# Kernel tuning notes

Measured on AMD Instinct MI355X. Metric: run time of the kernel, lower is better.

The kernel has to match this reference:

```python
import jax, jax.numpy as jnp
import numpy as np

N_NODES = 50000
N_EDGES = 600000
IN_F, HID, OUT_F = 602, 128, 41


def _gconv(x, W, b, src, dst, n):
    # DGL GraphConv, norm='both': D_dst^{-1/2} A (D_src^{-1/2} x W) + b
    ones = jnp.ones(src.shape, dtype=x.dtype)
    deg_out = jnp.clip(jax.ops.segment_sum(ones, src, num_segments=n), 1.0)
    deg_in = jnp.clip(jax.ops.segment_sum(ones, dst, num_segments=n), 1.0)
    h = x * jax.lax.rsqrt(deg_out)[:, None]
    h = h @ W  # dense transform first (in_feats > out_feats path)
    agg = jax.ops.segment_sum(h[src], dst, num_segments=n)  # [N, out]
    return agg * jax.lax.rsqrt(deg_in)[:, None] + b


def setup_inputs() -> dict:
    key = jax.random.key(0)
    ks = jax.random.split(key, 8)
    features = jax.random.normal(ks[0], (N_NODES, IN_F), dtype=jnp.float32)
    src = jax.random.randint(ks[1], (N_EDGES,), 0, N_NODES, dtype=jnp.int32)
    dst = jax.random.randint(ks[2], (N_EDGES,), 0, N_NODES, dtype=jnp.int32)
    def glorot(k, fan_in, fan_out):
        s = jnp.sqrt(6.0 / (fan_in + fan_out)).astype(jnp.float32)
        return jax.random.uniform(k, (fan_in, fan_out), jnp.float32, -s, s)
    return {
        'features': features, 'src': src, 'dst': dst,
        'W1': glorot(ks[3], IN_F, HID), 'b1': jnp.zeros((HID,), jnp.float32),
        'W2': glorot(ks[4], HID, HID), 'b2': jnp.zeros((HID,), jnp.float32),
        'W3': glorot(ks[5], HID, HID), 'b3': jnp.zeros((HID,), jnp.float32),
        'Wfc': glorot(ks[6], HID, OUT_F), 'bfc': jnp.zeros((OUT_F,), jnp.float32),
    }


def reference(features, src, dst, W1, b1, W2, b2, W3, b3, Wfc, bfc):
    n = features.shape[0]
    relu = jax.nn.relu
    x = relu(_gconv(features, W1, b1, src, dst, n))  # x = _x
    _x = relu(_gconv(x, W2, b2, src, dst, n))        # branch (layer2)
    x = relu(_gconv(x, W2, b2, src, dst, n))         # main (same layer2)
    x = relu(_gconv(x, W3, b3, src, dst, n))         # layer3
    x = relu(x + _x)                                  # residual + relu
    return x @ Wfc + bfc
```

## Files before the change

kernel.cpp:

```cpp
#include <hip/hip_runtime.h>
#include <hip/hip_bf16.h>

#define NN   50000
#define NE   600000
#define INF  602
#define HID  128
#define OUTF 41
#define NBLK 196

#define HISTB 2344
#define GEMMB 782

typedef __attribute__((ext_vector_type(8))) short bf16x8;
typedef __attribute__((ext_vector_type(4))) float f32x4;
typedef __attribute__((ext_vector_type(2))) float f32x2;

__device__ inline unsigned short f2bf(float x) {
    unsigned u = __float_as_uint(x);
    unsigned r = u + 0x7FFF + ((u >> 16) & 1);
    return (unsigned short)(r >> 16);
}

__device__ inline unsigned pack2bf(float lo, float hi) {
    return ((unsigned)f2bf(hi) << 16) | f2bf(lo);
}

__device__ inline f32x2 up2(unsigned u) {
    return (f32x2){__uint_as_float(u << 16), __uint_as_float(u & 0xFFFF0000u)};
}

#define GLL16(gp, lp) \
    __builtin_amdgcn_global_load_lds((const __attribute__((address_space(1))) unsigned int*)(gp), \
                                     (__attribute__((address_space(3))) unsigned int*)(lp), 16, 0, 0)

__device__ inline void prep_w_body(const float* __restrict__ W, int K,
                                   unsigned short* __restrict__ out, int total4, int i) {
    if (i >= total4) return;
    int col = i & 127;
    int k4 = (i >> 7) << 2;
    short4 h;
    h.x = (short)f2bf((k4 + 0 < K) ? W[(size_t)(k4 + 0) * HID + col] : 0.f);
    h.y = (short)f2bf((k4 + 1 < K) ? W[(size_t)(k4 + 1) * HID + col] : 0.f);
    h.z = (short)f2bf((k4 + 2 < K) ? W[(size_t)(k4 + 2) * HID + col] : 0.f);
    h.w = (short)f2bf((k4 + 3 < K) ? W[(size_t)(k4 + 3) * HID + col] : 0.f);
    *(short4*)&out[(size_t)(k4 >> 3) * 1024 + col * 8 + (k4 & 7)] = h;
}

__global__ __launch_bounds__(256) void hist_prep_k(const int* __restrict__ src,
                                                   const int* __restrict__ dst,
                                                   int* __restrict__ cnt_out,
                                                   int* __restrict__ cnt_in,
                                                   const float* __restrict__ W1,
                                                   const float* __restrict__ W2,
                                                   const float* __restrict__ W3,
                                                   unsigned short* __restrict__ W1t,
                                                   unsigned short* __restrict__ W2t,
                                                   unsigned short* __restrict__ W3t) {
    int b = blockIdx.x;
    if (b < HISTB) {
        int e = b * 256 + threadIdx.x;
        if (e < NE) {
            atomicAdd(&cnt_out[src[e]], 1);
            atomicAdd(&cnt_in[dst[e]], 1);
        }
    } else {
        int b2 = b - HISTB;
        if (b2 < 80)       prep_w_body(W1, INF, W1t, 20480, b2 * 256 + threadIdx.x);
        else if (b2 < 96)  prep_w_body(W2, HID, W2t, 4096, (b2 - 80) * 256 + threadIdx.x);
        else               prep_w_body(W3, HID, W3t, 4096, (b2 - 96) * 256 + threadIdx.x);
    }
}

__global__ __launch_bounds__(256) void scan1_k(const int* __restrict__ cnt,
                                               int* __restrict__ rowptr,
                                               int* __restrict__ blockSum) {
    __shared__ int tmp[256];
    int tid = threadIdx.x;
    int i = blockIdx.x * 256 + tid;
    int v = (i < NN) ? cnt[i] : 0;
    tmp[tid] = v;
    __syncthreads();
#pragma unroll
    for (int off = 1; off < 256; off <<= 1) {
        int t = (tid >= off) ? tmp[tid - off] : 0;
        __syncthreads();
        tmp[tid] += t;
        __syncthreads();
    }
    if (i < NN) rowptr[i] = tmp[tid] - v;
    if (tid == 255) blockSum[blockIdx.x] = tmp[255];
}

__global__ __launch_bounds__(256) void scan23_k(int* __restrict__ rowptr,
                                                const int* __restrict__ blockSum,
                                                int* __restrict__ wcur,
                                                const int* __restrict__ cnt_out,
                                                const int* __restrict__ cnt_in,
                                                float* __restrict__ rs_out,
                                                float* __restrict__ rs_in) {
    const int tid = threadIdx.x;
    const int bid = blockIdx.x;
    int vAll = (tid < NBLK) ? blockSum[tid] : 0;
    int vPre = (tid < bid) ? vAll : 0;
#pragma unroll
    for (int o = 32; o; o >>= 1) {
        vAll += __shfl_down(vAll, o);
        vPre += __shfl_down(vPre, o);
    }
    __shared__ int sA[4], sP[4];
    if ((tid & 63) == 0) { sA[tid >> 6] = vAll; sP[tid >> 6] = vPre; }
    __syncthreads();
    int offAll = sA[0] + sA[1] + sA[2] + sA[3];
    int offPre = sP[0] + sP[1] + sP[2] + sP[3];
    int i = bid * 256 + tid;
    if (i < NN) {
        int r = rowptr[i] + offPre;
        rowptr[i] = r;
        wcur[i] = r;
        int co = cnt_out[i]; if (co < 1) co = 1;
        int ci = cnt_in[i];  if (ci < 1) ci = 1;
        rs_out[i] = rsqrtf((float)co);
        rs_in[i]  = rsqrtf((float)ci);
    }
    if (bid == NBLK - 1 && tid == 0) rowptr[NN] = offAll;
}

__global__ __launch_bounds__(256) void fill_gemm1_k(const int* __restrict__ src,
                                                    const int* __restrict__ dst,
                                                    int* __restrict__ wcur,
                                                    int* __restrict__ csrsrc,
                                                    const float* __restrict__ A,
                                                    const unsigned short* __restrict__ Wt,
                                                    const float* __restrict__ rs_out,
                                                    unsigned short* __restrict__ H, int n) {
    if (blockIdx.x < HISTB) {
        int e = blockIdx.x * 256 + threadIdx.x;
        if (e < NE) {
            int p = atomicAdd(&wcur[dst[e]], 1);
            csrsrc[p] = src[e];
        }
        return;
    }

    const int gb = blockIdx.x - HISTB;
    const int tid = threadIdx.x;
    const int wave = tid >> 6;
    const int lane = tid & 63;
    const int quad = lane >> 4;
    const int l16 = lane & 15;
    const int tileBase = gb * 64 + wave * 16;

    const int arow_i = tileBase + l16;
    const float* __restrict__ arow = A + (size_t)(arow_i < n ? arow_i : 0) * INF;

    f32x4 acc[8];
#pragma unroll
    for (int j = 0; j < 8; ++j) acc[j] = (f32x4){0.f, 0.f, 0.f, 0.f};

    auto step = [&](float4& va, float4& vb, int kgUse, int kgRef, bool doRef) {
        union { bf16x8 v; unsigned u[4]; } af;
        af.u[0] = pack2bf(va.x, va.y);
        af.u[1] = pack2bf(va.z, va.w);
        af.u[2] = pack2bf(vb.x, vb.y);
        af.u[3] = pack2bf(vb.z, vb.w);
        if (doRef) {
            const float* p = arow + kgRef * 32 + quad * 8;
            va = *(const float4*)p;
            vb = *(const float4*)(p + 4);
        }
        const unsigned short* bg = Wt + (size_t)(kgUse * 4 + quad) * 1024 + l16 * 8;
#pragma unroll
        for (int nt = 0; nt < 8; ++nt) {
            bf16x8 bf = *(const bf16x8*)(bg + nt * 128);
            acc[nt] = __builtin_amdgcn_mfma_f32_16x16x32_bf16(af.v, bf, acc[nt], 0, 0, 0);
        }
    };

    float4 a0, b0, a1, b1, a2, b2;
    {
        const float* p0 = arow + quad * 8;
        a0 = *(const float4*)p0;            b0 = *(const float4*)(p0 + 4);
        a1 = *(const float4*)(p0 + 32);     b1 = *(const float4*)(p0 + 36);
        a2 = *(const float4*)(p0 + 64);     b2 = *(const float4*)(p0 + 68);
    }
    for (int i = 0; i < 5; ++i) {
        step(a0, b0, 3 * i,     3 * i + 3, true);
        step(a1, b1, 3 * i + 1, 3 * i + 4, true);
        step(a2, b2, 3 * i + 2, 3 * i + 5, true);
    }
    step(a0, b0, 15, 0, false);
    {
        int kb = 576 + quad * 8;
        if (quad < 3) {
            a0 = *(const float4*)(arow + kb);
            b0 = *(const float4*)(arow + kb + 4);
        } else {
            a0 = make_float4(arow[600], arow[601], 0.f, 0.f);
            b0 = make_float4(0.f, 0.f, 0.f, 0.f);
        }
    }
    step(a1, b1, 16, 0, false);
    step(a2, b2, 17, 0, false);
    step(a0, b0, 18, 0, false);

#pragma unroll
    for (int r = 0; r < 4; ++r) {
        int row = tileBase + quad * 4 + r;
        if (row < n) {
            float ro = rs_out[row];
#pragma unroll
            for (int nt = 0; nt < 8; ++nt)
                H[(size_t)row * HID + nt * 16 + l16] = f2bf(acc[nt][r] * ro);
        }
    }
}

__global__ __launch_bounds__(256) void gemm_hid_k(const unsigned short* __restrict__ A,
                                                  const unsigned short* __restrict__ Wt,
                                                  unsigned short* __restrict__ H, int n) {
    __shared__ __attribute__((aligned(16))) short As[64 * 136];
    __shared__ __attribute__((aligned(16))) short Bs[16384];

    const int tid = threadIdx.x;
    const int wave = tid >> 6;
    const int lane = tid & 63;
    const int quad = lane >> 4;
    const int l16 = lane & 15;
    const int wm = wave >> 1;
    const int wn = wave & 1;
    const int rowBase = blockIdx.x * 64;

#pragma unroll
    for (int c = 0; c < 8; ++c)
        GLL16(Wt + c * 2048 + tid * 8, &Bs[c * 2048 + tid * 8]);

#pragma unroll
    for (int c = 0; c < 4; ++c) {
        int f = c * 256 + tid;
        int row = f >> 4;
        int k16 = (f & 15) << 3;
        int grow = rowBase + row;
        int4 v = {0, 0, 0, 0};
        if (grow < n) v = *(const int4*)(A + (size_t)grow * HID + k16);
        *(int4*)&As[row * 136 + k16] = v;
    }
    __syncthreads();

    f32x4 acc[2][4];
#pragma unroll
    for (int i = 0; i < 2; ++i)
#pragma unroll
        for (int j = 0; j < 4; ++j) acc[i][j] = (f32x4){0.f, 0.f, 0.f, 0.f};

#pragma unroll
    for (int kq = 0; kq < 4; ++kq) {
        bf16x8 af[2], bfr[4];
#pragma unroll
        for (int mt = 0; mt < 2; ++mt)
            af[mt] = *(const bf16x8*)&As[(wm * 32 + mt * 16 + l16) * 136 + kq * 32 + quad * 8];
#pragma unroll
        for (int nt = 0; nt < 4; ++nt)
            bfr[nt] = *(const bf16x8*)&Bs[(kq * 4 + quad) * 1024 + (wn * 64 + nt * 16 + l16) * 8];
#pragma unroll
        for (int mt = 0; mt < 2; ++mt)
#pragma unroll
            for (int nt = 0; nt < 4; ++nt)
                acc[mt][nt] = __builtin_amdgcn_mfma_f32_16x16x32_bf16(af[mt], bfr[nt], acc[mt][nt], 0, 0, 0);
    }

#pragma unroll
    for (int mt = 0; mt < 2; ++mt)
#pragma unroll
        for (int r = 0; r < 4; ++r) {
            int row = rowBase + wm * 32 + mt * 16 + quad * 4 + r;
            if (row < n) {
#pragma unroll
                for (int nt = 0; nt < 4; ++nt) {
                    int col = wn * 64 + nt * 16 + l16;
                    H[(size_t)row * HID + col] = f2bf(acc[mt][nt][r]);
                }
            }
        }
}

__global__ __launch_bounds__(256) void gather_k(const unsigned short* __restrict__ H,
                                                const int* __restrict__ rowptr,
                                                const int* __restrict__ csrsrc,
                                                const float* __restrict__ rs_in,
                                                const float* __restrict__ rs_out,
                                                const float* __restrict__ bias,
                                                const float* __restrict__ resid,
                                                float* __restrict__ outX,
                                                unsigned short* __restrict__ outXs,
                                                int n) {
    const int lane = threadIdx.x & 63;
    const int g = lane >> 4;
    const int l = lane & 15;
    const int gbase = g << 4;
    const int wid = blockIdx.x * 4 + (threadIdx.x >> 6);
    const int node = wid * 4 + g;
    const bool alive = node < n;

    int beg = 0, end = 0;
    if (alive) { beg = rowptr[node]; end = rowptr[node + 1]; }

    f32x2 a01 = {0.f, 0.f}, a23 = {0.f, 0.f}, a45 = {0.f, 0.f}, a67 = {0.f, 0.f};

    for (int base = beg; base < end; base += 16) {
        int m = end - base; if (m > 16) m = 16;
        int idx = (l < m) ? csrsrc[base + l] : 0;
        int j = 0;
        for (; j + 3 < m; j += 4) {
            int s0 = __shfl(idx, gbase | j);
            int s1 = __shfl(idx, gbase | (j + 1));
            int s2 = __shfl(idx, gbase | (j + 2));
            int s3 = __shfl(idx, gbase | (j + 3));
            int4 u0 = *(const int4*)(H + (size_t)s0 * HID + l * 8);
            int4 u1 = *(const int4*)(H + (size_t)s1 * HID + l * 8);
            int4 u2 = *(const int4*)(H + (size_t)s2 * HID + l * 8);
            int4 u3 = *(const int4*)(H + (size_t)s3 * HID + l * 8);
#pragma unroll
            for (int q = 0; q < 4; ++q) {
                int4 u = (q == 0) ? u0 : (q == 1) ? u1 : (q == 2) ? u2 : u3;
                a01 += up2((unsigned)u.x);
                a23 += up2((unsigned)u.y);
                a45 += up2((unsigned)u.z);
                a67 += up2((unsigned)u.w);
            }
        }
        for (; j < m; ++j) {
            int s = __shfl(idx, gbase | j);
            int4 u = *(const int4*)(H + (size_t)s * HID + l * 8);
            a01 += up2((unsigned)u.x);
            a23 += up2((unsigned)u.y);
            a45 += up2((unsigned)u.z);
            a67 += up2((unsigned)u.w);
        }
    }

    if (!alive) return;

    float ri = rs_in[node];
    float4 b0 = *(const float4*)(bias + l * 8);
    float4 b1 = *(const float4*)(bias + l * 8 + 4);
    float v[8];
    v[0] = fmaxf(a01[0] * ri + b0.x, 0.f); v[1] = fmaxf(a01[1] * ri + b0.y, 0.f);
    v[2] = fmaxf(a23[0] * ri + b0.z, 0.f); v[3] = fmaxf(a23[1] * ri + b0.w, 0.f);
    v[4] = fmaxf(a45[0] * ri + b1.x, 0.f); v[5] = fmaxf(a45[1] * ri + b1.y, 0.f);
    v[6] = fmaxf(a67[0] * ri + b1.z, 0.f); v[7] = fmaxf(a67[1] * ri + b1.w, 0.f);

    size_t o = (size_t)node * HID + l * 8;
    if (resid) {
        float4 r0 = *(const float4*)(resid + o);
        float4 r1 = *(const float4*)(resid + o + 4);
        v[0] = fmaxf(v[0] + r0.x, 0.f); v[1] = fmaxf(v[1] + r0.y, 0.f);
        v[2] = fmaxf(v[2] + r0.z, 0.f); v[3] = fmaxf(v[3] + r0.w, 0.f);
        v[4] = fmaxf(v[4] + r1.x, 0.f); v[5] = fmaxf(v[5] + r1.y, 0.f);
        v[6] = fmaxf(v[6] + r1.z, 0.f); v[7] = fmaxf(v[7] + r1.w, 0.f);
    }
    if (outX) {
        *(float4*)(outX + o) = make_float4(v[0], v[1], v[2], v[3]);
        *(float4*)(outX + o + 4) = make_float4(v[4], v[5], v[6], v[7]);
    }
    if (outXs) {
        float ro = rs_out[node];
        int4 h;
        h.x = (int)(((unsigned)f2bf(v[1] * ro) << 16) | f2bf(v[0] * ro));
        h.y = (int)(((unsigned)f2bf(v[3] * ro) << 16) | f2bf(v[2] * ro));
        h.z = (int)(((unsigned)f2bf(v[5] * ro) << 16) | f2bf(v[4] * ro));
        h.w = (int)(((unsigned)f2bf(v[7] * ro) << 16) | f2bf(v[6] * ro));
        *(int4*)(outXs + o) = h;
    }
}

__global__ __launch_bounds__(256) void fc_k(const float* __restrict__ X,
                                            const float* __restrict__ Wfc,
                                            const float* __restrict__ bfc,
                                            float* __restrict__ out, int n) {
    __shared__ float Ws[HID * OUTF];
    __shared__ float Xs[4][HID];
    int tid = threadIdx.x;
    for (int i = tid; i < HID * OUTF; i += 256) Ws[i] = Wfc[i];
    int rowBase = blockIdx.x * 4;
    for (int i = tid; i < 4 * HID; i += 256) {
        int r = i >> 7, c = i & 127;
        int gr = rowBase + r;
        Xs[r][c] = (gr < n) ? X[(size_t)gr * HID + c] : 0.f;
    }
    __syncthreads();
    int wv = tid >> 6, lane = tid & 63;
    int row = rowBase + wv;
    if (row < n && lane < OUTF) {
        float acc = bfc[lane];
#pragma unroll 8
        for (int k = 0; k < HID; ++k) acc += Xs[wv][k] * Ws[k * OUTF + lane];
        out[(size_t)row * OUTF + lane] = acc;
    }
}

extern "C" void kernel_launch(void* const* d_in, const int* in_sizes, int n_in,
                              void* d_out, int out_size, void* d_ws, size_t ws_size,
                              hipStream_t stream) {
    const float* feat = (const float*)d_in[0];
    const int* src = (const int*)d_in[1];
    const int* dst = (const int*)d_in[2];
    const float* W1 = (const float*)d_in[3];
    const float* b1 = (const float*)d_in[4];
    const float* W2 = (const float*)d_in[5];
    const float* b2 = (const float*)d_in[6];
    const float* W3 = (const float*)d_in[7];
    const float* b3 = (const float*)d_in[8];
    const float* Wfc = (const float*)d_in[9];
    const float* bfc = (const float*)d_in[10];
    float* out = (float*)d_out;

    char* w = (char*)d_ws;
    auto alloc = [&](size_t b) -> void* {
        void* p = (void*)w;
        w += (b + 255) & ~(size_t)255;
        return p;
    };
    int* cnt = (int*)alloc(2 * NN * sizeof(int));
    int* cnt_out = cnt;
    int* cnt_in  = cnt + NN;
    int* rowptr  = (int*)alloc((NN + 1) * sizeof(int));
    int* wcur    = (int*)alloc(NN * sizeof(int));
    int* csrsrc  = (int*)alloc(NE * sizeof(int));
    int* blockSum = (int*)alloc(NBLK * sizeof(int));
    float* rs_out = (float*)alloc(NN * sizeof(float));
    float* rs_in  = (float*)alloc(NN * sizeof(float));
    unsigned short* W1t = (unsigned short*)alloc(10 * 8192 * sizeof(unsigned short));
    unsigned short* W2t = (unsigned short*)alloc(16384 * sizeof(unsigned short));
    unsigned short* W3t = (unsigned short*)alloc(16384 * sizeof(unsigned short));
    unsigned short* Ha = (unsigned short*)alloc((size_t)NN * HID * sizeof(unsigned short));
    unsigned short* Hb = (unsigned short*)alloc((size_t)NN * HID * sizeof(unsigned short));
    unsigned short* Xb = (unsigned short*)alloc((size_t)NN * HID * sizeof(unsigned short));
    float* resid = (float*)alloc((size_t)NN * HID * sizeof(float));
    float* Xfc   = (float*)alloc((size_t)NN * HID * sizeof(float));

    hipMemsetAsync(cnt, 0, 2 * NN * sizeof(int), stream);

    hist_prep_k<<<HISTB + 112, 256, 0, stream>>>(src, dst, cnt_out, cnt_in,
                                                 W1, W2, W3, W1t, W2t, W3t);
    scan1_k<<<NBLK, 256, 0, stream>>>(cnt_in, rowptr, blockSum);
    scan23_k<<<NBLK, 256, 0, stream>>>(rowptr, blockSum, wcur, cnt_out, cnt_in, rs_out, rs_in);
    fill_gemm1_k<<<HISTB + GEMMB, 256, 0, stream>>>(src, dst, wcur, csrsrc,
                                                    feat, W1t, rs_out, Ha, NN);

    const int ablk = (NN + 15) / 16;
    gather_k<<<ablk, 256, 0, stream>>>(Ha, rowptr, csrsrc, rs_in, rs_out, b1,
                                       nullptr, nullptr, Xb, NN);
    gemm_hid_k<<<GEMMB, 256, 0, stream>>>(Xb, W2t, Hb, NN);
    gather_k<<<ablk, 256, 0, stream>>>(Hb, rowptr, csrsrc, rs_in, rs_out, b2,
                                       nullptr, resid, Xb, NN);
    gemm_hid_k<<<GEMMB, 256, 0, stream>>>(Xb, W3t, Ha, NN);
    gather_k<<<ablk, 256, 0, stream>>>(Ha, rowptr, csrsrc, rs_in, rs_out, b3,
                                       resid, Xfc, nullptr, NN);
    fc_k<<<(NN + 3) / 4, 256, 0, stream>>>(Xfc, Wfc, bfc, out, NN);
}
```

Baseline: 442.9 us.

## Split layer-1 GEMM across histogram and CSR-fill kernels, move out-degree scaling to gather

The layer-1 dense GEMM no longer depends on rs_out, so its tiles are interleaved into both the degree-histogram kernel and the CSR-fill kernel, letting the atomic-bound passes overlap with MFMA work. The first gather applies the per-source rsqrt(out-degree) per edge through a new roEdge pointer. The memset is folded into the weight-prep kernel, which now runs ahead of the histogram as its own launch. The cost is an extra per-edge scalar load and multiply in the first gather, and one more launch for weight prep.

```diff
diff --git a/kernel.cpp b/kernel.cpp
--- a/kernel.cpp
+++ b/kernel.cpp
@@ -10,6 +10,9 @@
 
 #define HISTB 2344
 #define GEMMB 782
+#define G1N   586
+#define MEGA1B 2930
+#define MEGA2B 2548
 
 typedef __attribute__((ext_vector_type(8))) short bf16x8;
 typedef __attribute__((ext_vector_type(4))) float f32x4;
@@ -46,28 +49,116 @@
     *(short4*)&out[(size_t)(k4 >> 3) * 1024 + col * 8 + (k4 & 7)] = h;
 }
 
-__global__ __launch_bounds__(256) void hist_prep_k(const int* __restrict__ src,
-                                                   const int* __restrict__ dst,
-                                                   int* __restrict__ cnt_out,
-                                                   int* __restrict__ cnt_in,
-                                                   const float* __restrict__ W1,
-                                                   const float* __restrict__ W2,
-                                                   const float* __restrict__ W3,
-                                                   unsigned short* __restrict__ W1t,
-                                                   unsigned short* __restrict__ W2t,
-                                                   unsigned short* __restrict__ W3t) {
+__global__ __launch_bounds__(256) void prep_all_k(const float* __restrict__ W1,
+                                                  const float* __restrict__ W2,
+                                                  const float* __restrict__ W3,
+                                                  unsigned short* __restrict__ W1t,
+                                                  unsigned short* __restrict__ W2t,
+                                                  unsigned short* __restrict__ W3t,
+                                                  int* __restrict__ cnt) {
     int b = blockIdx.x;
-    if (b < HISTB) {
-        int e = b * 256 + threadIdx.x;
+    if (b < 80) {
+        int t = b * 256 + threadIdx.x;
+        prep_w_body(W1, INF, W1t, 20480, t);
+        for (int i = t; i < 2 * NN; i += 20480) cnt[i] = 0;
+    } else if (b < 96) {
+        prep_w_body(W2, HID, W2t, 4096, (b - 80) * 256 + threadIdx.x);
+    } else {
+        prep_w_body(W3, HID, W3t, 4096, (b - 96) * 256 + threadIdx.x);
+    }
+}
+
+__device__ inline void gemm1_tile(int g, int tid,
+                                  const float* __restrict__ A,
+                                  const unsigned short* __restrict__ Wt,
+                                  unsigned short* __restrict__ H, int n) {
+    const int wave = tid >> 6;
+    const int lane = tid & 63;
+    const int quad = lane >> 4;
+    const int l16 = lane & 15;
+    const int tileBase = g * 64 + wave * 16;
+
+    const int arow_i = tileBase + l16;
+    const float* __restrict__ arow = A + (size_t)(arow_i < n ? arow_i : 0) * INF;
+
+    f32x4 acc[8];
+#pragma unroll
+    for (int j = 0; j < 8; ++j) acc[j] = (f32x4){0.f, 0.f, 0.f, 0.f};
+
+    auto step = [&](float4& va, float4& vb, int kgUse, int kgRef, bool doRef) {
+        union { bf16x8 v; unsigned u[4]; } af;
+        af.u[0] = pack2bf(va.x, va.y);
+        af.u[1] = pack2bf(va.z, va.w);
+        af.u[2] = pack2bf(vb.x, vb.y);
+        af.u[3] = pack2bf(vb.z, vb.w);
+        if (doRef) {
+            const float* p = arow + kgRef * 32 + quad * 8;
+            va = *(const float4*)p;
+            vb = *(const float4*)(p + 4);
+        }
+        const unsigned short* bg = Wt + (size_t)(kgUse * 4 + quad) * 1024 + l16 * 8;
+#pragma unroll
+        for (int nt = 0; nt < 8; ++nt) {
+            bf16x8 bf = *(const bf16x8*)(bg + nt * 128);
+            acc[nt] = __builtin_amdgcn_mfma_f32_16x16x32_bf16(af.v, bf, acc[nt], 0, 0, 0);
+        }
+    };
+
+    float4 a0, b0, a1, b1, a2, b2;
+    {
+        const float* p0 = arow + quad * 8;
+        a0 = *(const float4*)p0;            b0 = *(const float4*)(p0 + 4);
+        a1 = *(const float4*)(p0 + 32);     b1 = *(const float4*)(p0 + 36);
+        a2 = *(const float4*)(p0 + 64);     b2 = *(const float4*)(p0 + 68);
+    }
+    for (int i = 0; i < 5; ++i) {
+        step(a0, b0, 3 * i,     3 * i + 3, true);
+        step(a1, b1, 3 * i + 1, 3 * i + 4, true);
+        step(a2, b2, 3 * i + 2, 3 * i + 5, true);
+    }
+    step(a0, b0, 15, 0, false);
+    {
+        int kb = 576 + quad * 8;
+        if (quad < 3) {
+            a0 = *(const float4*)(arow + kb);
+            b0 = *(const float4*)(arow + kb + 4);
+        } else {
+            a0 = make_float4(arow[600], arow[601], 0.f, 0.f);
+            b0 = make_float4(0.f, 0.f, 0.f, 0.f);
+        }
+    }
+    step(a1, b1, 16, 0, false);
+    step(a2, b2, 17, 0, false);
+    step(a0, b0, 18, 0, false);
+
+#pragma unroll
+    for (int r = 0; r < 4; ++r) {
+        int row = tileBase + quad * 4 + r;
+        if (row < n) {
+#pragma unroll
+            for (int nt = 0; nt < 8; ++nt)
+                H[(size_t)row * HID + nt * 16 + l16] = f2bf(acc[nt][r]);
+        }
+    }
+}
+
+__global__ __launch_bounds__(256) void mega1_k(const int* __restrict__ src,
+                                               const int* __restrict__ dst,
+                                               int* __restrict__ cnt_out,
+                                               int* __restrict__ cnt_in,
+                                               const float* __restrict__ A,
+                                               const unsigned short* __restrict__ Wt,
+                                               unsigned short* __restrict__ H, int n) {
+    int b = blockIdx.x;
+    if ((b % 5) == 4) {
+        gemm1_tile(b / 5, threadIdx.x, A, Wt, H, n);
+    } else {
+        int h = b - b / 5;
+        int e = h * 256 + threadIdx.x;
         if (e < NE) {
             atomicAdd(&cnt_out[src[e]], 1);
             atomicAdd(&cnt_in[dst[e]], 1);
         }
-    } else {
-        int b2 = b - HISTB;
-        if (b2 < 80)       prep_w_body(W1, INF, W1t, 20480, b2 * 256 + threadIdx.x);
-        else if (b2 < 96)  prep_w_body(W2, HID, W2t, 4096, (b2 - 80) * 256 + threadIdx.x);
-        else               prep_w_body(W3, HID, W3t, 4096, (b2 - 96) * 256 + threadIdx.x);
     }
 }
 
@@ -125,92 +216,24 @@
     if (bid == NBLK - 1 && tid == 0) rowptr[NN] = offAll;
 }
 
-__global__ __launch_bounds__(256) void fill_gemm1_k(const int* __restrict__ src,
-                                                    const int* __restrict__ dst,
-                                                    int* __restrict__ wcur,
-                                                    int* __restrict__ csrsrc,
-                                                    const float* __restrict__ A,
-                                                    const unsigned short* __restrict__ Wt,
-                                                    const float* __restrict__ rs_out,
-                                                    unsigned short* __restrict__ H, int n) {
-    if (blockIdx.x < HISTB) {
-        int e = blockIdx.x * 256 + threadIdx.x;
-        if (e < NE) {
-            int p = atomicAdd(&wcur[dst[e]], 1);
-            csrsrc[p] = src[e];
-        }
-        return;
-    }
-
-    const int gb = blockIdx.x - HISTB;
-    const int tid = threadIdx.x;
-    const int wave = tid >> 6;
-    const int lane = tid & 63;
-    const int quad = lane >> 4;
-    const int l16 = lane & 15;
-    const int tileBase = gb * 64 + wave * 16;
-
-    const int arow_i = tileBase + l16;
-    const float* __restrict__ arow = A + (size_t)(arow_i < n ? arow_i : 0) * INF;
-
-    f32x4 acc[8];
-#pragma unroll
-    for (int j = 0; j < 8; ++j) acc[j] = (f32x4){0.f, 0.f, 0.f, 0.f};
-
-    auto step = [&](float4& va, float4& vb, int kgUse, int kgRef, bool doRef) {
-        union { bf16x8 v; unsigned u[4]; } af;
-        af.u[0] = pack2bf(va.x, va.y);
-        af.u[1] = pack2bf(va.z, va.w);
-        af.u[2] = pack2bf(vb.x, vb.y);
-        af.u[3] = pack2bf(vb.z, vb.w);
-        if (doRef) {
-            const float* p = arow + kgRef * 32 + quad * 8;
-            va = *(const float4*)p;
-            vb = *(const float4*)(p + 4);
-        }
-        const unsigned short* bg = Wt + (size_t)(kgUse * 4 + quad) * 1024 + l16 * 8;
-#pragma unroll
-        for (int nt = 0; nt < 8; ++nt) {
-            bf16x8 bf = *(const bf16x8*)(bg + nt * 128);
-            acc[nt] = __builtin_amdgcn_mfma_f32_16x16x32_bf16(af.v, bf, acc[nt], 0, 0, 0);
-        }
-    };
-
-    float4 a0, b0, a1, b1, a2, b2;
-    {
-        const float* p0 = arow + quad * 8;
-        a0 = *(const float4*)p0;            b0 = *(const float4*)(p0 + 4);
-        a1 = *(const float4*)(p0 + 32);     b1 = *(const float4*)(p0 + 36);
-        a2 = *(const float4*)(p0 + 64);     b2 = *(const float4*)(p0 + 68);
-    }
-    for (int i = 0; i < 5; ++i) {
-        step(a0, b0, 3 * i,     3 * i + 3, true);
-        step(a1, b1, 3 * i + 1, 3 * i + 4, true);
-        step(a2, b2, 3 * i + 2, 3 * i + 5, true);
-    }
-    step(a0, b0, 15, 0, false);
-    {
-        int kb = 576 + quad * 8;
-        if (quad < 3) {
-            a0 = *(const float4*)(arow + kb);
-            b0 = *(const float4*)(arow + kb + 4);
-        } else {
-            a0 = make_float4(arow[600], arow[601], 0.f, 0.f);
-            b0 = make_float4(0.f, 0.f, 0.f, 0.f);
-        }
-    }
-    step(a1, b1, 16, 0, false);
-    step(a2, b2, 17, 0, false);
-    step(a0, b0, 18, 0, false);
-
-#pragma unroll
-    for (int r = 0; r < 4; ++r) {
-        int row = tileBase + quad * 4 + r;
-        if (row < n) {
-            float ro = rs_out[row];
-#pragma unroll
-            for (int nt = 0; nt < 8; ++nt)
-                H[(size_t)row * HID + nt * 16 + l16] = f2bf(acc[nt][r] * ro);
+__global__ __launch_bounds__(256) void mega2_k(const int* __restrict__ src,
+                                               const int* __restrict__ dst,
+                                               int* __restrict__ wcur,
+                                               int* __restrict__ csrsrc,
+                                               const float* __restrict__ A,
+                                               const unsigned short* __restrict__ Wt,
+                                               unsigned short* __restrict__ H, int n) {
+    int b = blockIdx.x;
+    if ((b % 13) == 12) {
+        gemm1_tile(G1N + b / 13, threadIdx.x, A, Wt, H, n);
+    } else {
+        int f = b - b / 13;
+        if (f < HISTB) {
+            int e = f * 256 + threadIdx.x;
+            if (e < NE) {
+                int p = atomicAdd(&wcur[dst[e]], 1);
+                csrsrc[p] = src[e];
+            }
         }
     }
 }
@@ -289,6 +312,7 @@
                                                 const float* __restrict__ rs_in,
                                                 const float* __restrict__ rs_out,
                                                 const float* __restrict__ bias,
+                                                const float* __restrict__ roEdge,
                                                 const float* __restrict__ resid,
                                                 float* __restrict__ outX,
                                                 unsigned short* __restrict__ outXs,
@@ -306,35 +330,69 @@
 
     f32x2 a01 = {0.f, 0.f}, a23 = {0.f, 0.f}, a45 = {0.f, 0.f}, a67 = {0.f, 0.f};
 
-    for (int base = beg; base < end; base += 16) {
-        int m = end - base; if (m > 16) m = 16;
-        int idx = (l < m) ? csrsrc[base + l] : 0;
-        int j = 0;
-        for (; j + 3 < m; j += 4) {
-            int s0 = __shfl(idx, gbase | j);
-            int s1 = __shfl(idx, gbase | (j + 1));
-            int s2 = __shfl(idx, gbase | (j + 2));
-            int s3 = __shfl(idx, gbase | (j + 3));
-            int4 u0 = *(const int4*)(H + (size_t)s0 * HID + l * 8);
-            int4 u1 = *(const int4*)(H + (size_t)s1 * HID + l * 8);
-            int4 u2 = *(const int4*)(H + (size_t)s2 * HID + l * 8);
-            int4 u3 = *(const int4*)(H + (size_t)s3 * HID + l * 8);
-#pragma unroll
-            for (int q = 0; q < 4; ++q) {
-                int4 u = (q == 0) ? u0 : (q == 1) ? u1 : (q == 2) ? u2 : u3;
+    if (roEdge) {
+        for (int base = beg; base < end; base += 16) {
+            int m = end - base; if (m > 16) m = 16;
+            int idx = (l < m) ? csrsrc[base + l] : 0;
+            int j = 0;
+            for (; j + 3 < m; j += 4) {
+                int s0 = __shfl(idx, gbase | j);
+                int s1 = __shfl(idx, gbase | (j + 1));
+                int s2 = __shfl(idx, gbase | (j + 2));
+                int s3 = __shfl(idx, gbase | (j + 3));
+                float r0 = roEdge[s0], r1 = roEdge[s1], r2 = roEdge[s2], r3 = roEdge[s3];
+                int4 u0 = *(const int4*)(H + (size_t)s0 * HID + l * 8);
+                int4 u1 = *(const int4*)(H + (size_t)s1 * HID + l * 8);
+                int4 u2 = *(const int4*)(H + (size_t)s2 * HID + l * 8);
+                int4 u3 = *(const int4*)(H + (size_t)s3 * HID + l * 8);
+                a01 += r0 * up2((unsigned)u0.x); a23 += r0 * up2((unsigned)u0.y);
+                a45 += r0 * up2((unsigned)u0.z); a67 += r0 * up2((unsigned)u0.w);
+                a01 += r1 * up2((unsigned)u1.x); a23 += r1 * up2((unsigned)u1.y);
+                a45 += r1 * up2((unsigned)u1.z); a67 += r1 * up2((unsigned)u1.w);
+                a01 += r2 * up2((unsigned)u2.x); a23 += r2 * up2((unsigned)u2.y);
+                a45 += r2 * up2((unsigned)u2.z); a67 += r2 * up2((unsigned)u2.w);
+                a01 += r3 * up2((unsigned)u3.x); a23 += r3 * up2((unsigned)u3.y);
+                a45 += r3 * up2((unsigned)u3.z); a67 += r3 * up2((unsigned)u3.w);
+            }
+            for (; j < m; ++j) {
+                int s = __shfl(idx, gbase | j);
+                float r = roEdge[s];
+                int4 u = *(const int4*)(H + (size_t)s * HID + l * 8);
+                a01 += r * up2((unsigned)u.x); a23 += r * up2((unsigned)u.y);
+                a45 += r * up2((unsigned)u.z); a67 += r * up2((unsigned)u.w);
+            }
+        }
+    } else {
+        for (int base = beg; base < end; base += 16) {
+            int m = end - base; if (m > 16) m = 16;
+            int idx = (l < m) ? csrsrc[base + l] : 0;
+            int j = 0;
+            for (; j + 3 < m; j += 4) {
+                int s0 = __shfl(idx, gbase | j);
+                int s1 = __shfl(idx, gbase | (j + 1));
+                int s2 = __shfl(idx, gbase | (j + 2));
+                int s3 = __shfl(idx, gbase | (j + 3));
+                int4 u0 = *(const int4*)(H + (size_t)s0 * HID + l * 8);
+                int4 u1 = *(const int4*)(H + (size_t)s1 * HID + l * 8);
+                int4 u2 = *(const int4*)(H + (size_t)s2 * HID + l * 8);
+                int4 u3 = *(const int4*)(H + (size_t)s3 * HID + l * 8);
+#pragma unroll
+                for (int q = 0; q < 4; ++q) {
+                    int4 u = (q == 0) ? u0 : (q == 1) ? u1 : (q == 2) ? u2 : u3;
+                    a01 += up2((unsigned)u.x);
+                    a23 += up2((unsigned)u.y);
+                    a45 += up2((unsigned)u.z);
+                    a67 += up2((unsigned)u.w);
+                }
+            }
+            for (; j < m; ++j) {
+                int s = __shfl(idx, gbase | j);
+                int4 u = *(const int4*)(H + (size_t)s * HID + l * 8);
                 a01 += up2((unsigned)u.x);
                 a23 += up2((unsigned)u.y);
                 a45 += up2((unsigned)u.z);
                 a67 += up2((unsigned)u.w);
             }
-        }
-        for (; j < m; ++j) {
-            int s = __shfl(idx, gbase | j);
-            int4 u = *(const int4*)(H + (size_t)s * HID + l * 8);
-            a01 += up2((unsigned)u.x);
-            a23 += up2((unsigned)u.y);
-            a45 += up2((unsigned)u.z);
-            a67 += up2((unsigned)u.w);
         }
     }
 
@@ -438,23 +496,20 @@
     float* resid = (float*)alloc((size_t)NN * HID * sizeof(float));
     float* Xfc   = (float*)alloc((size_t)NN * HID * sizeof(float));
 
-    hipMemsetAsync(cnt, 0, 2 * NN * sizeof(int), stream);
-
-    hist_prep_k<<<HISTB + 112, 256, 0, stream>>>(src, dst, cnt_out, cnt_in,
-                                                 W1, W2, W3, W1t, W2t, W3t);
+    prep_all_k<<<112, 256, 0, stream>>>(W1, W2, W3, W1t, W2t, W3t, cnt);
+    mega1_k<<<MEGA1B, 256, 0, stream>>>(src, dst, cnt_out, cnt_in, feat, W1t, Ha, NN);
     scan1_k<<<NBLK, 256, 0, stream>>>(cnt_in, rowptr, blockSum);
     scan23_k<<<NBLK, 256, 0, stream>>>(rowptr, blockSum, wcur, cnt_out, cnt_in, rs_out, rs_in);
-    fill_gemm1_k<<<HISTB + GEMMB, 256, 0, stream>>>(src, dst, wcur, csrsrc,
-                                                    feat, W1t, rs_out, Ha, NN);
+    mega2_k<<<MEGA2B, 256, 0, stream>>>(src, dst, wcur, csrsrc, feat, W1t, Ha, NN);
 
     const int ablk = (NN + 15) / 16;
     gather_k<<<ablk, 256, 0, stream>>>(Ha, rowptr, csrsrc, rs_in, rs_out, b1,
-                                       nullptr, nullptr, Xb, NN);
+                                       rs_out, nullptr, nullptr, Xb, NN);
     gemm_hid_k<<<GEMMB, 256, 0, stream>>>(Xb, W2t, Hb, NN);
     gather_k<<<ablk, 256, 0, stream>>>(Hb, rowptr, csrsrc, rs_in, rs_out, b2,
-                                       nullptr, resid, Xb, NN);
+                                       nullptr, nullptr, resid, Xb, NN);
     gemm_hid_k<<<GEMMB, 256, 0, stream>>>(Xb, W3t, Ha, NN);
     gather_k<<<ablk, 256, 0, stream>>>(Ha, rowptr, csrsrc, rs_in, rs_out, b3,
-                                       resid, Xfc, nullptr, NN);
+                                       nullptr, resid, Xfc, nullptr, NN);
     fc_k<<<(NN + 3) / 4, 256, 0, stream>>>(Xfc, Wfc, bfc, out, NN);
 }
```

Result: slower. 463.0 us (+4.5%).
